# Kernel tuning notes

Measured on AMD Instinct MI355X. Metric: run time of the kernel, lower is better.

Reference implementation:

```python
import jax, jax.numpy as jnp
import numpy as np

N = 100000   # n_nodes
E = 1600000  # n_edges (avg degree 16)
IN, HID, OUT = 128, 128, 64


def setup_inputs() -> dict:
    key = jax.random.key(0)
    k0, k1, k2, k3 = jax.random.split(key, 4)
    x = jax.random.normal(k0, (N, IN), dtype=jnp.float32)
    edge_index = jax.random.randint(k1, (2, E), 0, N, dtype=jnp.int32)
    # Glorot-ish init for GCNConv weights, zero bias (PyG default bias=True)
    W1 = jax.random.normal(k2, (IN, HID), dtype=jnp.float32) * (1.0 / np.sqrt(IN))
    b1 = jnp.zeros((HID,), dtype=jnp.float32)
    W2 = jax.random.normal(k3, (HID, OUT), dtype=jnp.float32) * (1.0 / np.sqrt(HID))
    b2 = jnp.zeros((OUT,), dtype=jnp.float32)
    return {"x": x, "W1": W1, "b1": b1, "W2": W2, "b2": b2, "edge_index": edge_index}


def gcn_layer(x, W, b, src, dst):
    """PyG GCNConv: add self-loops, symmetric deg^{-1/2} normalization,
    linear transform, scatter-add aggregation at dst, plus bias."""
    n = x.shape[0]
    h = x @ W                                   # [n, d_out]
    loops = jnp.arange(n, dtype=src.dtype)
    s = jnp.concatenate([src, loops])           # sources incl. self-loops
    d = jnp.concatenate([dst, loops])           # targets incl. self-loops
    deg = jax.ops.segment_sum(jnp.ones_like(d, dtype=h.dtype), d, num_segments=n)
    dinv = jnp.where(deg > 0, jax.lax.rsqrt(deg), 0.0)
    norm = dinv[s] * dinv[d]                    # [E+n]
    msg = h[s] * norm[:, None]                  # gather + scale
    out = jax.ops.segment_sum(msg, d, num_segments=n)  # scatter-add
    return out + b


def reference(x, W1, b1, W2, b2, edge_index):
    src, dst = edge_index[0], edge_index[1]
    h = jax.nn.relu(gcn_layer(x, W1, b1, src, dst))
    return gcn_layer(h, W2, b2, src, dst)
```

## Files before the change

kernel.cpp:

```cpp
#include <hip/hip_runtime.h>

#define NNODES 100000
#define NEDGES 1600000
#define IND 128
#define HIDD 128
#define OUTD 64

#define BSHIFT 9
#define BSIZE  512
#define NBUCK  ((NNODES + BSIZE - 1) / BSIZE)
#define SLACK  9216
#define BIN_EPB  8192
#define SEG_CAP  10240
#define BINB   ((NEDGES + BIN_EPB - 1) / BIN_EPB)
#define WTB    ((IND * HIDD + HIDD * OUTD + 255) / 256)

typedef unsigned int  uint32;
typedef __attribute__((ext_vector_type(8))) short short8;
typedef __attribute__((ext_vector_type(4))) float floatx4;
typedef __attribute__((ext_vector_type(4))) unsigned int uivec4;
typedef __attribute__((ext_vector_type(4))) float fvec4;

__device__ __forceinline__ unsigned short f2bf(float f) {
    union { float f; uint32 u; } x; x.f = f;
    uint32 u = x.u;
    return (unsigned short)((u + 0x7fffu + ((u >> 16) & 1u)) >> 16);
}
__device__ __forceinline__ float bflo(uint32 u) {
    union { uint32 i; float f; } x; x.i = u << 16; return x.f;
}
__device__ __forceinline__ float bfhi(uint32 u) {
    union { uint32 i; float f; } x; x.i = u & 0xffff0000u; return x.f;
}

__global__ void k_bin(const int* __restrict__ src, const int* __restrict__ dst,
                      int* __restrict__ bcnt, uint32* __restrict__ staging, int e,
                      const float* __restrict__ W1, const float* __restrict__ W2,
                      unsigned short* __restrict__ wt1, unsigned short* __restrict__ wt2) {
    const int tid = threadIdx.x;
    if (blockIdx.x >= BINB) {
        int idx = (blockIdx.x - BINB) * 256 + tid;
        if (idx < IND * HIDD) {
            int k = idx / HIDD, m = idx - k * HIDD;
            wt1[m * IND + k] = f2bf(W1[idx]);
        } else {
            int j = idx - IND * HIDD;
            if (j < HIDD * OUTD) {
                int k = j / OUTD, m = j - k * OUTD;
                wt2[m * HIDD + k] = f2bf(W2[j]);
            }
        }
        return;
    }

    __shared__ int lh[NBUCK];
    __shared__ int lcur[NBUCK];
    for (int i = tid; i < NBUCK; i += 256) lh[i] = 0;
    __syncthreads();

    int start = blockIdx.x * BIN_EPB;
    int end = min(start + BIN_EPB, e);

    for (int i = start + tid; i < end; i += 256)
        atomicAdd(&lh[dst[i] >> BSHIFT], 1);
    __syncthreads();

    for (int i = tid; i < NBUCK; i += 256)
        lcur[i] = lh[i] ? atomicAdd(&bcnt[i], lh[i]) : 0;
    __syncthreads();

    for (int i = start + tid; i < end; i += 256) {
        int d = dst[i], s = src[i];
        int b = d >> BSHIFT;
        int pos = atomicAdd(&lcur[b], 1);
        if (pos < SLACK)
            staging[b * SLACK + pos] = ((uint32)(d & (BSIZE - 1)) << 17) | (uint32)s;
    }
}

__global__ void k_fill3(const uint32* __restrict__ staging, const int* __restrict__ bcnt,
                        int* __restrict__ row_ptr, int* __restrict__ csr_src,
                        float* __restrict__ dinv, int n) {
    __shared__ int nc[BSIZE];
    __shared__ int lcur[BSIZE];
    __shared__ int sbuf[256];
    __shared__ int boffl[NBUCK + 1];
    __shared__ int seg[SEG_CAP];
    const int b = blockIdx.x;
    const int base = b << BSHIFT;
    const int tid = threadIdx.x;
    const int nn = min(BSIZE, n - base);

    for (int i = tid; i < BSIZE; i += 256) nc[i] = 0;

    int vb = (tid < NBUCK) ? bcnt[tid] : 0;
    sbuf[tid] = vb;
    __syncthreads();
    for (int off = 1; off < 256; off <<= 1) {
        int t = (tid >= off) ? sbuf[tid - off] : 0;
        __syncthreads();
        sbuf[tid] += t;
        __syncthreads();
    }
    if (tid < NBUCK) boffl[tid] = sbuf[tid] - vb;
    if (tid == 255) boffl[NBUCK] = sbuf[255];
    __syncthreads();

    const uint32* st = staging + (size_t)b * SLACK;
    const int cnt = bcnt[b];
    for (int i = tid; i < cnt; i += 256)
        atomicAdd(&nc[st[i] >> 17], 1);
    __syncthreads();

    int a0 = nc[2 * tid], a1 = nc[2 * tid + 1];
    sbuf[tid] = a0 + a1;
    __syncthreads();
    for (int off = 1; off < 256; off <<= 1) {
        int t = (tid >= off) ? sbuf[tid - off] : 0;
        __syncthreads();
        sbuf[tid] += t;
        __syncthreads();
    }
    int ex = sbuf[tid] - (a0 + a1);
    const int r0 = boffl[b];
    if (2 * tid < nn) {
        row_ptr[base + 2 * tid] = r0 + ex;
        dinv[base + 2 * tid] = rsqrtf((float)(a0 + 1));
    }
    if (2 * tid + 1 < nn) {
        row_ptr[base + 2 * tid + 1] = r0 + ex + a0;
        dinv[base + 2 * tid + 1] = rsqrtf((float)(a1 + 1));
    }
    lcur[2 * tid] = ex;
    lcur[2 * tid + 1] = ex + a0;
    if (b == (int)gridDim.x - 1 && tid == 255) row_ptr[n] = boffl[NBUCK];
    __syncthreads();

    for (int i = tid; i < cnt; i += 256) {
        uint32 p = st[i];
        int dl = (int)(p >> 17);
        int s  = (int)(p & 0x1FFFFu);
        int pos = atomicAdd(&lcur[dl], 1);
        if (pos < SEG_CAP) seg[pos] = s;
        else               csr_src[r0 + pos] = s;
    }
    __syncthreads();
    int lim = min(cnt, SEG_CAP);
    for (int i = tid; i < lim; i += 256) csr_src[r0 + i] = seg[i];
}

template<int K, int M, bool ABF16>
__launch_bounds__(512)
__global__ void gemm_mfma(const void* __restrict__ Ap, const unsigned short* __restrict__ WT,
                          const float* __restrict__ dinv, unsigned short* __restrict__ C, int n) {
    constexpr int KP = K + 8;
    constexpr int NT = M / 16;
    __shared__ unsigned short Asl[128 * KP];
    __shared__ unsigned short Wsl[M * KP];

    const int tid = threadIdx.x;
    const int row0 = blockIdx.x * 128;

    {
        constexpr int SEG = (K * 2) / 16;
        const uint4* srcp = (const uint4*)WT;
        for (int idx = tid; idx < M * SEG; idx += 512) {
            int r = idx / SEG, s = idx - r * SEG;
            *(uint4*)(Wsl + r * KP + s * 8) = srcp[idx];
        }
    }
    if constexpr (ABF16) {
        constexpr int U4R = K / 8;
        const unsigned short* Ab = (const unsigned short*)Ap;
        for (int idx = tid; idx < 128 * U4R; idx += 512) {
            int r = idx / U4R, s = idx - r * U4R;
            int grow = row0 + r; if (grow >= n) grow = n - 1;
            *(uint4*)(Asl + r * KP + s * 8) = *(const uint4*)(Ab + (size_t)grow * K + s * 8);
        }
    } else {
        constexpr int F4R = K / 4;
        const float* Af = (const float*)Ap;
        for (int idx = tid; idx < 128 * F4R; idx += 512) {
            int r = idx / F4R, s = idx - r * F4R;
            int grow = row0 + r; if (grow >= n) grow = n - 1;
            float4 v = *(const float4*)(Af + (size_t)grow * K + s * 4);
            uint32 p0 = (uint32)f2bf(v.x) | ((uint32)f2bf(v.y) << 16);
            uint32 p1 = (uint32)f2bf(v.z) | ((uint32)f2bf(v.w) << 16);
            *(uint2*)(Asl + r * KP + s * 4) = make_uint2(p0, p1);
        }
    }
    __syncthreads();

    const int lane = tid & 63;
    const int wave = tid >> 6;
    const int mm = lane & 15;
    const int qq = lane >> 4;

    floatx4 acc[NT];
#pragma unroll
    for (int t = 0; t < NT; t++) acc[t] = (floatx4){0.f, 0.f, 0.f, 0.f};

#pragma unroll
    for (int kc = 0; kc < K / 32; kc++) {
        short8 a = *(const short8*)(Asl + (wave * 16 + mm) * KP + kc * 32 + qq * 8);
#pragma unroll
        for (int t = 0; t < NT; t++) {
            short8 b = *(const short8*)(Wsl + (t * 16 + mm) * KP + kc * 32 + qq * 8);
            acc[t] = __builtin_amdgcn_mfma_f32_16x16x32_bf16(a, b, acc[t], 0, 0, 0);
        }
    }

#pragma unroll
    for (int r = 0; r < 4; r++) {
        int grow = row0 + wave * 16 + qq * 4 + r;
        if (grow < n) {
            float dv = dinv[grow];
#pragma unroll
            for (int t = 0; t < NT; t++)
                C[(size_t)grow * M + t * 16 + mm] = f2bf(acc[t][r] * dv);
        }
    }
}

__launch_bounds__(256)
__global__ void gather_gemm(const unsigned short* __restrict__ h,
                            const int* __restrict__ row_ptr,
                            const int* __restrict__ csr_src,
                            const float* __restrict__ dinv,
                            const float* __restrict__ bias1,
                            const unsigned short* __restrict__ WT2,
                            unsigned short* __restrict__ C2, int n) {
    constexpr int K  = HIDD;
    constexpr int KP = K + 8;
    constexpr int M2 = OUTD;
    __shared__ unsigned short Atl[16 * KP];
    __shared__ unsigned short Wsl[M2 * KP];

    const int tid = threadIdx.x;

    {
        constexpr int SEG = (K * 2) / 16;
        const uint4* srcp = (const uint4*)WT2;
        for (int idx = tid; idx < M2 * SEG; idx += 256) {
            int r = idx / SEG, s = idx - r * SEG;
            *(uint4*)(Wsl + r * KP + s * 8) = srcp[idx];
        }
    }

    const int g = tid >> 4;
    const int l = tid & 15;
    const int v0 = blockIdx.x * 16;
    const int v = v0 + g;

    uint4 pk = make_uint4(0u, 0u, 0u, 0u);
    if (v < n) {
        const float dv = dinv[v];
        float acc[8];
        {
            uint4 u = *(const uint4*)(h + (size_t)v * K + l * 8);
            acc[0] = bflo(u.x); acc[1] = bfhi(u.x);
            acc[2] = bflo(u.y); acc[3] = bfhi(u.y);
            acc[4] = bflo(u.z); acc[5] = bfhi(u.z);
            acc[6] = bflo(u.w); acc[7] = bfhi(u.w);
        }

        int j   = row_ptr[v];
        int end = row_ptr[v + 1];
        for (; j + 3 < end; j += 4) {
            int s0 = csr_src[j];
            int s1 = csr_src[j + 1];
            int s2 = csr_src[j + 2];
            int s3 = csr_src[j + 3];
            uint4 u0 = *(const uint4*)(h + (size_t)s0 * K + l * 8);
            uint4 u1 = *(const uint4*)(h + (size_t)s1 * K + l * 8);
            uint4 u2 = *(const uint4*)(h + (size_t)s2 * K + l * 8);
            uint4 u3 = *(const uint4*)(h + (size_t)s3 * K + l * 8);
            acc[0] += (bflo(u0.x) + bflo(u1.x)) + (bflo(u2.x) + bflo(u3.x));
            acc[1] += (bfhi(u0.x) + bfhi(u1.x)) + (bfhi(u2.x) + bfhi(u3.x));
            acc[2] += (bflo(u0.y) + bflo(u1.y)) + (bflo(u2.y) + bflo(u3.y));
            acc[3] += (bfhi(u0.y) + bfhi(u1.y)) + (bfhi(u2.y) + bfhi(u3.y));
            acc[4] += (bflo(u0.z) + bflo(u1.z)) + (bflo(u2.z) + bflo(u3.z));
            acc[5] += (bfhi(u0.z) + bfhi(u1.z)) + (bfhi(u2.z) + bfhi(u3.z));
            acc[6] += (bflo(u0.w) + bflo(u1.w)) + (bflo(u2.w) + bflo(u3.w));
            acc[7] += (bfhi(u0.w) + bfhi(u1.w)) + (bfhi(u2.w) + bfhi(u3.w));
        }
        for (; j < end; j++) {
            int s0 = csr_src[j];
            uint4 u0 = *(const uint4*)(h + (size_t)s0 * K + l * 8);
            acc[0] += bflo(u0.x); acc[1] += bfhi(u0.x);
            acc[2] += bflo(u0.y); acc[3] += bfhi(u0.y);
            acc[4] += bflo(u0.z); acc[5] += bfhi(u0.z);
            acc[6] += bflo(u0.w); acc[7] += bfhi(u0.w);
        }

#pragma unroll
        for (int i = 0; i < 8; i++) {
            acc[i] = fmaxf(acc[i] * dv + bias1[l * 8 + i], 0.0f);
        }
        pk.x = (uint32)f2bf(acc[0]) | ((uint32)f2bf(acc[1]) << 16);
        pk.y = (uint32)f2bf(acc[2]) | ((uint32)f2bf(acc[3]) << 16);
        pk.z = (uint32)f2bf(acc[4]) | ((uint32)f2bf(acc[5]) << 16);
        pk.w = (uint32)f2bf(acc[6]) | ((uint32)f2bf(acc[7]) << 16);
    }
    *(uint4*)(Atl + g * KP + l * 8) = pk;
    __syncthreads();

    const int lane = tid & 63;
    const int wv = tid >> 6;
    const int mm = lane & 15;
    const int qq = lane >> 4;

    floatx4 o = (floatx4){0.f, 0.f, 0.f, 0.f};
#pragma unroll
    for (int kc = 0; kc < K / 32; kc++) {
        short8 a = *(const short8*)(Atl + mm * KP + kc * 32 + qq * 8);
        short8 b = *(const short8*)(Wsl + (wv * 16 + mm) * KP + kc * 32 + qq * 8);
        o = __builtin_amdgcn_mfma_f32_16x16x32_bf16(a, b, o, 0, 0, 0);
    }

#pragma unroll
    for (int r = 0; r < 4; r++) {
        int grow = v0 + qq * 4 + r;
        if (grow < n) {
            float dv2 = dinv[grow];
            C2[(size_t)grow * M2 + wv * 16 + mm] = f2bf(o[r] * dv2);
        }
    }
}

template<int M, bool RELU, bool OBF16>
__launch_bounds__(256)
__global__ void gather_k(const unsigned short* __restrict__ h,
                         const int* __restrict__ row_ptr,
                         const int* __restrict__ csr_src,
                         const float* __restrict__ dinv,
                         const float* __restrict__ bias,
                         void* __restrict__ outp, int n) {
    constexpr int LPG = M / 8;
    constexpr int GPB = 256 / LPG;
    const int g = threadIdx.x / LPG;
    const int l = threadIdx.x % LPG;
    const int v = blockIdx.x * GPB + g;
    if (v >= n) return;

    const float dv = dinv[v];
    float acc[8];
    {
        uint4 u = *(const uint4*)(h + (size_t)v * M + l * 8);
        acc[0] = bflo(u.x); acc[1] = bfhi(u.x);
        acc[2] = bflo(u.y); acc[3] = bfhi(u.y);
        acc[4] = bflo(u.z); acc[5] = bfhi(u.z);
        acc[6] = bflo(u.w); acc[7] = bfhi(u.w);
    }

    int j   = row_ptr[v];
    int end = row_ptr[v + 1];
    for (; j + 3 < end; j += 4) {
        int s0 = csr_src[j];
        int s1 = csr_src[j + 1];
        int s2 = csr_src[j + 2];
        int s3 = csr_src[j + 3];
        uint4 u0 = *(const uint4*)(h + (size_t)s0 * M + l * 8);
        uint4 u1 = *(const uint4*)(h + (size_t)s1 * M + l * 8);
        uint4 u2 = *(const uint4*)(h + (size_t)s2 * M + l * 8);
        uint4 u3 = *(const uint4*)(h + (size_t)s3 * M + l * 8);
        acc[0] += (bflo(u0.x) + bflo(u1.x)) + (bflo(u2.x) + bflo(u3.x));
        acc[1] += (bfhi(u0.x) + bfhi(u1.x)) + (bfhi(u2.x) + bfhi(u3.x));
        acc[2] += (bflo(u0.y) + bflo(u1.y)) + (bflo(u2.y) + bflo(u3.y));
        acc[3] += (bfhi(u0.y) + bfhi(u1.y)) + (bfhi(u2.y) + bfhi(u3.y));
        acc[4] += (bflo(u0.z) + bflo(u1.z)) + (bflo(u2.z) + bflo(u3.z));
        acc[5] += (bfhi(u0.z) + bfhi(u1.z)) + (bfhi(u2.z) + bfhi(u3.z));
        acc[6] += (bflo(u0.w) + bflo(u1.w)) + (bflo(u2.w) + bflo(u3.w));
        acc[7] += (bfhi(u0.w) + bfhi(u1.w)) + (bfhi(u2.w) + bfhi(u3.w));
    }
    for (; j < end; j++) {
        int s0 = csr_src[j];
        uint4 u0 = *(const uint4*)(h + (size_t)s0 * M + l * 8);
        acc[0] += bflo(u0.x); acc[1] += bfhi(u0.x);
        acc[2] += bflo(u0.y); acc[3] += bfhi(u0.y);
        acc[4] += bflo(u0.z); acc[5] += bfhi(u0.z);
        acc[6] += bflo(u0.w); acc[7] += bfhi(u0.w);
    }

#pragma unroll
    for (int i = 0; i < 8; i++) {
        acc[i] = acc[i] * dv + bias[l * 8 + i];
        if (RELU) acc[i] = fmaxf(acc[i], 0.0f);
    }

    if constexpr (OBF16) {
        uivec4 p;
#pragma unroll
        for (int c = 0; c < 4; c++)
            p[c] = (uint32)f2bf(acc[2 * c]) | ((uint32)f2bf(acc[2 * c + 1]) << 16);
        __builtin_nontemporal_store(p,
            (uivec4*)((unsigned short*)outp + (size_t)v * M + l * 8));
    } else {
        float* op = (float*)outp + (size_t)v * M + l * 8;
        fvec4 a0 = {acc[0], acc[1], acc[2], acc[3]};
        fvec4 a1 = {acc[4], acc[5], acc[6], acc[7]};
        __builtin_nontemporal_store(a0, (fvec4*)op);
        __builtin_nontemporal_store(a1, (fvec4*)(op + 4));
    }
}

extern "C" void kernel_launch(void* const* d_in, const int* in_sizes, int n_in,
                              void* d_out, int out_size, void* d_ws, size_t ws_size,
                              hipStream_t stream) {
    const float* x  = (const float*)d_in[0];
    const float* W1 = (const float*)d_in[1];
    const float* b1 = (const float*)d_in[2];
    const float* W2 = (const float*)d_in[3];
    const float* b2 = (const float*)d_in[4];
    const int*   ei = (const int*)d_in[5];
    const int* src = ei;
    const int* dst = ei + NEDGES;
    float* out = (float*)d_out;

    char* ws = (char*)d_ws;
    float*  dinv    = (float*)ws;   ws += (size_t)NNODES * 4;
    int*    row_ptr = (int*)ws;     ws += (size_t)(NNODES + 4) * 4;
    int*    bcnt    = (int*)ws;     ws += 256 * 4;
    int*    boff    = (int*)ws;     ws += 260 * 4;
    unsigned short* wt1 = (unsigned short*)ws;  ws += (size_t)IND * HIDD * 2;
    unsigned short* wt2 = (unsigned short*)ws;  ws += (size_t)HIDD * OUTD * 2;
    int*    csr_src = (int*)ws;     ws += (size_t)NEDGES * 4;
    uint32* staging = (uint32*)ws;  ws += (size_t)NBUCK * SLACK * 4;
    unsigned short* hbf1 = (unsigned short*)ws; ws += (size_t)NNODES * HIDD * 2;
    unsigned short* hbf2 = (unsigned short*)ws;

    hipMemsetAsync(bcnt, 0, 256 * 4, stream);
    k_bin<<<BINB + WTB, 256, 0, stream>>>(src, dst, bcnt, staging, NEDGES, W1, W2, wt1, wt2);
    k_fill3<<<NBUCK, 256, 0, stream>>>(staging, bcnt, row_ptr, csr_src, dinv, NNODES);

    gemm_mfma<IND, HIDD, false><<<(NNODES + 127) / 128, 512, 0, stream>>>(
        x, wt1, dinv, hbf1, NNODES);

    gather_gemm<<<(NNODES + 15) / 16, 256, 0, stream>>>(
        hbf1, row_ptr, csr_src, dinv, b1, wt2, hbf2, NNODES);

    gather_k<OUTD, false, false><<<(NNODES * (OUTD / 8) + 255) / 256, 256, 0, stream>>>(
        hbf2, row_ptr, csr_src, dinv, b2, out, NNODES);
}
```

Baseline: 306.9 us.

## Replace bucketed CSR build with global-atomic degree count and fuse scatter into GEMM

The two-pass bucket binning (staging buffer plus per-bucket shared-memory sort) is replaced by a per-node global atomic degree count, a block-wise row_ptr scan, and a cursor-based scatter into csr_src. The scatter blocks are launched in the same grid as the first-layer MFMA GEMM, so edge scatter overlaps the dense transform. This removes the staging buffer's write and re-read. In exchange it relies on heavily contended global atomics with random destinations, and the order of neighbours within each row becomes nondeterministic.

```diff
diff --git a/kernel.cpp b/kernel.cpp
--- a/kernel.cpp
+++ b/kernel.cpp
@@ -9,11 +9,14 @@
 #define BSHIFT 9
 #define BSIZE  512
 #define NBUCK  ((NNODES + BSIZE - 1) / BSIZE)
-#define SLACK  9216
-#define BIN_EPB  8192
-#define SEG_CAP  10240
-#define BINB   ((NEDGES + BIN_EPB - 1) / BIN_EPB)
+
+#define DEG_EPB 4096
+#define DEGB   ((NEDGES + DEG_EPB - 1) / DEG_EPB)
 #define WTB    ((IND * HIDD + HIDD * OUTD + 255) / 256)
+
+#define SCB    784
+#define SC_EPB ((NEDGES + SCB - 1) / SCB)
+#define GEMMB  ((NNODES + 127) / 128)
 
 typedef unsigned int  uint32;
 typedef __attribute__((ext_vector_type(8))) short short8;
@@ -33,13 +36,13 @@
     union { uint32 i; float f; } x; x.i = u & 0xffff0000u; return x.f;
 }
 
-__global__ void k_bin(const int* __restrict__ src, const int* __restrict__ dst,
-                      int* __restrict__ bcnt, uint32* __restrict__ staging, int e,
+__global__ void k_deg(const int* __restrict__ dst, int* __restrict__ deg,
+                      int* __restrict__ bsum, int e,
                       const float* __restrict__ W1, const float* __restrict__ W2,
                       unsigned short* __restrict__ wt1, unsigned short* __restrict__ wt2) {
     const int tid = threadIdx.x;
-    if (blockIdx.x >= BINB) {
-        int idx = (blockIdx.x - BINB) * 256 + tid;
+    if (blockIdx.x >= DEGB) {
+        int idx = (blockIdx.x - DEGB) * 256 + tid;
         if (idx < IND * HIDD) {
             int k = idx / HIDD, m = idx - k * HIDD;
             wt1[m * IND + k] = f2bf(W1[idx]);
@@ -54,112 +57,85 @@
     }
 
     __shared__ int lh[NBUCK];
-    __shared__ int lcur[NBUCK];
     for (int i = tid; i < NBUCK; i += 256) lh[i] = 0;
     __syncthreads();
 
-    int start = blockIdx.x * BIN_EPB;
-    int end = min(start + BIN_EPB, e);
-
-    for (int i = start + tid; i < end; i += 256)
-        atomicAdd(&lh[dst[i] >> BSHIFT], 1);
-    __syncthreads();
-
+    int start = blockIdx.x * DEG_EPB;
+    int end = min(start + DEG_EPB, e);
+    for (int i = start + tid; i < end; i += 256) {
+        int d = dst[i];
+        atomicAdd(&deg[d], 1);
+        atomicAdd(&lh[d >> BSHIFT], 1);
+    }
+    __syncthreads();
     for (int i = tid; i < NBUCK; i += 256)
-        lcur[i] = lh[i] ? atomicAdd(&bcnt[i], lh[i]) : 0;
-    __syncthreads();
-
-    for (int i = start + tid; i < end; i += 256) {
-        int d = dst[i], s = src[i];
-        int b = d >> BSHIFT;
-        int pos = atomicAdd(&lcur[b], 1);
-        if (pos < SLACK)
-            staging[b * SLACK + pos] = ((uint32)(d & (BSIZE - 1)) << 17) | (uint32)s;
-    }
-}
-
-__global__ void k_fill3(const uint32* __restrict__ staging, const int* __restrict__ bcnt,
-                        int* __restrict__ row_ptr, int* __restrict__ csr_src,
-                        float* __restrict__ dinv, int n) {
-    __shared__ int nc[BSIZE];
-    __shared__ int lcur[BSIZE];
-    __shared__ int sbuf[256];
-    __shared__ int boffl[NBUCK + 1];
-    __shared__ int seg[SEG_CAP];
+        if (lh[i]) atomicAdd(&bsum[i], lh[i]);
+}
+
+__global__ __launch_bounds__(512)
+void k_rowptr(const int* __restrict__ deg, const int* __restrict__ bsum,
+              int* __restrict__ row_ptr, int* __restrict__ cursor,
+              float* __restrict__ dinv, int n) {
+    __shared__ int sb[512];
     const int b = blockIdx.x;
-    const int base = b << BSHIFT;
     const int tid = threadIdx.x;
-    const int nn = min(BSIZE, n - base);
-
-    for (int i = tid; i < BSIZE; i += 256) nc[i] = 0;
-
-    int vb = (tid < NBUCK) ? bcnt[tid] : 0;
-    sbuf[tid] = vb;
-    __syncthreads();
-    for (int off = 1; off < 256; off <<= 1) {
-        int t = (tid >= off) ? sbuf[tid - off] : 0;
+
+    sb[tid] = (tid < b) ? bsum[tid] : 0;
+    __syncthreads();
+    for (int off = 256; off > 0; off >>= 1) {
+        if (tid < off) sb[tid] += sb[tid + off];
         __syncthreads();
-        sbuf[tid] += t;
+    }
+    const int base_off = sb[0];
+    __syncthreads();
+
+    const int v = (b << BSHIFT) + tid;
+    int dg = (v < n) ? deg[v] : 0;
+    sb[tid] = dg;
+    __syncthreads();
+    for (int off = 1; off < 512; off <<= 1) {
+        int t = (tid >= off) ? sb[tid - off] : 0;
         __syncthreads();
-    }
-    if (tid < NBUCK) boffl[tid] = sbuf[tid] - vb;
-    if (tid == 255) boffl[NBUCK] = sbuf[255];
-    __syncthreads();
-
-    const uint32* st = staging + (size_t)b * SLACK;
-    const int cnt = bcnt[b];
-    for (int i = tid; i < cnt; i += 256)
-        atomicAdd(&nc[st[i] >> 17], 1);
-    __syncthreads();
-
-    int a0 = nc[2 * tid], a1 = nc[2 * tid + 1];
-    sbuf[tid] = a0 + a1;
-    __syncthreads();
-    for (int off = 1; off < 256; off <<= 1) {
-        int t = (tid >= off) ? sbuf[tid - off] : 0;
+        sb[tid] += t;
         __syncthreads();
-        sbuf[tid] += t;
-        __syncthreads();
-    }
-    int ex = sbuf[tid] - (a0 + a1);
-    const int r0 = boffl[b];
-    if (2 * tid < nn) {
-        row_ptr[base + 2 * tid] = r0 + ex;
-        dinv[base + 2 * tid] = rsqrtf((float)(a0 + 1));
-    }
-    if (2 * tid + 1 < nn) {
-        row_ptr[base + 2 * tid + 1] = r0 + ex + a0;
-        dinv[base + 2 * tid + 1] = rsqrtf((float)(a1 + 1));
-    }
-    lcur[2 * tid] = ex;
-    lcur[2 * tid + 1] = ex + a0;
-    if (b == (int)gridDim.x - 1 && tid == 255) row_ptr[n] = boffl[NBUCK];
-    __syncthreads();
-
-    for (int i = tid; i < cnt; i += 256) {
-        uint32 p = st[i];
-        int dl = (int)(p >> 17);
-        int s  = (int)(p & 0x1FFFFu);
-        int pos = atomicAdd(&lcur[dl], 1);
-        if (pos < SEG_CAP) seg[pos] = s;
-        else               csr_src[r0 + pos] = s;
-    }
-    __syncthreads();
-    int lim = min(cnt, SEG_CAP);
-    for (int i = tid; i < lim; i += 256) csr_src[r0 + i] = seg[i];
-}
-
-template<int K, int M, bool ABF16>
+    }
+    int ex = sb[tid] - dg;
+    if (v < n) {
+        int rp = base_off + ex;
+        row_ptr[v] = rp;
+        cursor[v] = rp;
+        dinv[v] = rsqrtf((float)(dg + 1));
+        if (v == n - 1) row_ptr[n] = rp + dg;
+    }
+}
+
 __launch_bounds__(512)
-__global__ void gemm_mfma(const void* __restrict__ Ap, const unsigned short* __restrict__ WT,
-                          const float* __restrict__ dinv, unsigned short* __restrict__ C, int n) {
+__global__ void k_scatter_gemm(const int* __restrict__ src, const int* __restrict__ dst,
+                               int* __restrict__ cursor, int* __restrict__ csr_src, int e,
+                               const float* __restrict__ Af, const unsigned short* __restrict__ WT,
+                               const float* __restrict__ dinv, unsigned short* __restrict__ C, int n) {
+    constexpr int K = IND;
     constexpr int KP = K + 8;
+    constexpr int M = HIDD;
     constexpr int NT = M / 16;
     __shared__ unsigned short Asl[128 * KP];
     __shared__ unsigned short Wsl[M * KP];
 
     const int tid = threadIdx.x;
-    const int row0 = blockIdx.x * 128;
+    const int bid = blockIdx.x;
+
+    if (bid < SCB) {
+        int start = bid * SC_EPB;
+        int end = min(start + SC_EPB, e);
+        for (int i = start + tid; i < end; i += 512) {
+            int d = dst[i];
+            int pos = atomicAdd(&cursor[d], 1);
+            csr_src[pos] = src[i];
+        }
+        return;
+    }
+
+    const int row0 = (bid - SCB) * 128;
 
     {
         constexpr int SEG = (K * 2) / 16;
@@ -169,17 +145,8 @@
             *(uint4*)(Wsl + r * KP + s * 8) = srcp[idx];
         }
     }
-    if constexpr (ABF16) {
-        constexpr int U4R = K / 8;
-        const unsigned short* Ab = (const unsigned short*)Ap;
-        for (int idx = tid; idx < 128 * U4R; idx += 512) {
-            int r = idx / U4R, s = idx - r * U4R;
-            int grow = row0 + r; if (grow >= n) grow = n - 1;
-            *(uint4*)(Asl + r * KP + s * 8) = *(const uint4*)(Ab + (size_t)grow * K + s * 8);
-        }
-    } else {
+    {
         constexpr int F4R = K / 4;
-        const float* Af = (const float*)Ap;
         for (int idx = tid; idx < 128 * F4R; idx += 512) {
             int r = idx / F4R, s = idx - r * F4R;
             int grow = row0 + r; if (grow >= n) grow = n - 1;
@@ -420,21 +387,21 @@
     char* ws = (char*)d_ws;
     float*  dinv    = (float*)ws;   ws += (size_t)NNODES * 4;
     int*    row_ptr = (int*)ws;     ws += (size_t)(NNODES + 4) * 4;
-    int*    bcnt    = (int*)ws;     ws += 256 * 4;
-    int*    boff    = (int*)ws;     ws += 260 * 4;
+    int*    cursor  = (int*)ws;     ws += (size_t)NNODES * 4;
+    int*    deg     = (int*)ws;     ws += (size_t)NNODES * 4;
+    int*    bsum    = (int*)ws;     ws += 256 * 4;
     unsigned short* wt1 = (unsigned short*)ws;  ws += (size_t)IND * HIDD * 2;
     unsigned short* wt2 = (unsigned short*)ws;  ws += (size_t)HIDD * OUTD * 2;
     int*    csr_src = (int*)ws;     ws += (size_t)NEDGES * 4;
-    uint32* staging = (uint32*)ws;  ws += (size_t)NBUCK * SLACK * 4;
     unsigned short* hbf1 = (unsigned short*)ws; ws += (size_t)NNODES * HIDD * 2;
     unsigned short* hbf2 = (unsigned short*)ws;
 
-    hipMemsetAsync(bcnt, 0, 256 * 4, stream);
-    k_bin<<<BINB + WTB, 256, 0, stream>>>(src, dst, bcnt, staging, NEDGES, W1, W2, wt1, wt2);
-    k_fill3<<<NBUCK, 256, 0, stream>>>(staging, bcnt, row_ptr, csr_src, dinv, NNODES);
-
-    gemm_mfma<IND, HIDD, false><<<(NNODES + 127) / 128, 512, 0, stream>>>(
-        x, wt1, dinv, hbf1, NNODES);
+    hipMemsetAsync(deg, 0, (size_t)(NNODES + 256) * 4, stream);
+    k_deg<<<DEGB + WTB, 256, 0, stream>>>(dst, deg, bsum, NEDGES, W1, W2, wt1, wt2);
+    k_rowptr<<<NBUCK, 512, 0, stream>>>(deg, bsum, row_ptr, cursor, dinv, NNODES);
+
+    k_scatter_gemm<<<SCB + GEMMB, 512, 0, stream>>>(
+        src, dst, cursor, csr_src, NEDGES, x, wt1, dinv, hbf1, NNODES);
 
     gather_gemm<<<(NNODES + 15) / 16, 256, 0, stream>>>(
         hbf1, row_ptr, csr_src, dinv, b1, wt2, hbf2, NNODES);
```

Result: slower. 455.5 us (+48.4%).

## Fuse CSR fill with first GEMM via global degree atomics in binning

Applied to the files above, without the earlier changes.

The binning kernel now also counts per-node in-degree with global atomics, so the first GEMM can compute its deg^{-1/2} scaling directly instead of waiting for the CSR fill kernel. The CSR fill and the first GEMM are merged into one launch, with block ranges split between them and shared memory reused. The fill block size grows to 512 threads, one thread per node. This removes a kernel launch and a serialization point, letting fill and GEMM overlap, at the cost of 1.6M extra global atomics and a larger memset.

```diff
diff --git a/kernel.cpp b/kernel.cpp
--- a/kernel.cpp
+++ b/kernel.cpp
@@ -14,6 +14,7 @@
 #define SEG_CAP  10240
 #define BINB   ((NEDGES + BIN_EPB - 1) / BIN_EPB)
 #define WTB    ((IND * HIDD + HIDD * OUTD + 255) / 256)
+#define GEMMB  ((NNODES + 127) / 128)
 
 typedef unsigned int  uint32;
 typedef __attribute__((ext_vector_type(8))) short short8;
@@ -34,7 +35,8 @@
 }
 
 __global__ void k_bin(const int* __restrict__ src, const int* __restrict__ dst,
-                      int* __restrict__ bcnt, uint32* __restrict__ staging, int e,
+                      int* __restrict__ bcnt, int* __restrict__ deg,
+                      uint32* __restrict__ staging, int e,
                       const float* __restrict__ W1, const float* __restrict__ W2,
                       unsigned short* __restrict__ wt1, unsigned short* __restrict__ wt2) {
     const int tid = threadIdx.x;
@@ -61,8 +63,11 @@
     int start = blockIdx.x * BIN_EPB;
     int end = min(start + BIN_EPB, e);
 
-    for (int i = start + tid; i < end; i += 256)
-        atomicAdd(&lh[dst[i] >> BSHIFT], 1);
+    for (int i = start + tid; i < end; i += 256) {
+        int d = dst[i];
+        atomicAdd(&deg[d], 1);
+        atomicAdd(&lh[d >> BSHIFT], 1);
+    }
     __syncthreads();
 
     for (int i = tid; i < NBUCK; i += 256)
@@ -78,88 +83,88 @@
     }
 }
 
-__global__ void k_fill3(const uint32* __restrict__ staging, const int* __restrict__ bcnt,
-                        int* __restrict__ row_ptr, int* __restrict__ csr_src,
-                        float* __restrict__ dinv, int n) {
-    __shared__ int nc[BSIZE];
-    __shared__ int lcur[BSIZE];
-    __shared__ int sbuf[256];
-    __shared__ int boffl[NBUCK + 1];
-    __shared__ int seg[SEG_CAP];
-    const int b = blockIdx.x;
-    const int base = b << BSHIFT;
+__launch_bounds__(512)
+__global__ void k_fill_gemm(const uint32* __restrict__ staging, const int* __restrict__ bcnt,
+                            const int* __restrict__ deg,
+                            int* __restrict__ row_ptr, int* __restrict__ csr_src,
+                            float* __restrict__ dinv,
+                            const float* __restrict__ Af, const unsigned short* __restrict__ WT,
+                            unsigned short* __restrict__ C, int n) {
+    constexpr int K = IND;
+    constexpr int KP = K + 8;
+    constexpr int M = HIDD;
+    constexpr int NT = M / 16;
+    __shared__ __align__(16) char smem[(128 + 128) * KP * 2];
+
     const int tid = threadIdx.x;
-    const int nn = min(BSIZE, n - base);
-
-    for (int i = tid; i < BSIZE; i += 256) nc[i] = 0;
-
-    int vb = (tid < NBUCK) ? bcnt[tid] : 0;
-    sbuf[tid] = vb;
-    __syncthreads();
-    for (int off = 1; off < 256; off <<= 1) {
-        int t = (tid >= off) ? sbuf[tid - off] : 0;
-        __syncthreads();
-        sbuf[tid] += t;
-        __syncthreads();
-    }
-    if (tid < NBUCK) boffl[tid] = sbuf[tid] - vb;
-    if (tid == 255) boffl[NBUCK] = sbuf[255];
-    __syncthreads();
-
-    const uint32* st = staging + (size_t)b * SLACK;
-    const int cnt = bcnt[b];
-    for (int i = tid; i < cnt; i += 256)
-        atomicAdd(&nc[st[i] >> 17], 1);
-    __syncthreads();
-
-    int a0 = nc[2 * tid], a1 = nc[2 * tid + 1];
-    sbuf[tid] = a0 + a1;
-    __syncthreads();
-    for (int off = 1; off < 256; off <<= 1) {
-        int t = (tid >= off) ? sbuf[tid - off] : 0;
-        __syncthreads();
-        sbuf[tid] += t;
-        __syncthreads();
-    }
-    int ex = sbuf[tid] - (a0 + a1);
-    const int r0 = boffl[b];
-    if (2 * tid < nn) {
-        row_ptr[base + 2 * tid] = r0 + ex;
-        dinv[base + 2 * tid] = rsqrtf((float)(a0 + 1));
-    }
-    if (2 * tid + 1 < nn) {
-        row_ptr[base + 2 * tid + 1] = r0 + ex + a0;
-        dinv[base + 2 * tid + 1] = rsqrtf((float)(a1 + 1));
-    }
-    lcur[2 * tid] = ex;
-    lcur[2 * tid + 1] = ex + a0;
-    if (b == (int)gridDim.x - 1 && tid == 255) row_ptr[n] = boffl[NBUCK];
-    __syncthreads();
-
-    for (int i = tid; i < cnt; i += 256) {
-        uint32 p = st[i];
-        int dl = (int)(p >> 17);
-        int s  = (int)(p & 0x1FFFFu);
-        int pos = atomicAdd(&lcur[dl], 1);
-        if (pos < SEG_CAP) seg[pos] = s;
-        else               csr_src[r0 + pos] = s;
-    }
-    __syncthreads();
-    int lim = min(cnt, SEG_CAP);
-    for (int i = tid; i < lim; i += 256) csr_src[r0 + i] = seg[i];
-}
-
-template<int K, int M, bool ABF16>
-__launch_bounds__(512)
-__global__ void gemm_mfma(const void* __restrict__ Ap, const unsigned short* __restrict__ WT,
-                          const float* __restrict__ dinv, unsigned short* __restrict__ C, int n) {
-    constexpr int KP = K + 8;
-    constexpr int NT = M / 16;
-    __shared__ unsigned short Asl[128 * KP];
-    __shared__ unsigned short Wsl[M * KP];
-
-    const int tid = threadIdx.x;
-    const int row0 = blockIdx.x * 128;
+    const int bid = blockIdx.x;
+
+    if (bid < NBUCK) {
+        int* nc   = (int*)smem;
+        int* lcur = nc + 512;
+        int* sbuf = lcur + 512;
+        int* seg  = sbuf + 512;
+        const int b = bid;
+        const int base = b << BSHIFT;
+        const int v = base + tid;
+
+        nc[tid] = 0;
+
+        int vb = (tid < NBUCK) ? bcnt[tid] : 0;
+        sbuf[tid] = vb;
+        __syncthreads();
+        for (int off = 1; off < 512; off <<= 1) {
+            int t = (tid >= off) ? sbuf[tid - off] : 0;
+            __syncthreads();
+            sbuf[tid] += t;
+            __syncthreads();
+        }
+        const int r0    = (b > 0) ? sbuf[b - 1] : 0;
+        const int total = sbuf[NBUCK - 1];
+        __syncthreads();
+
+        const uint32* st = staging + (size_t)b * SLACK;
+        const int cnt = bcnt[b];
+        for (int i = tid; i < cnt; i += 512)
+            atomicAdd(&nc[st[i] >> 17], 1);
+        __syncthreads();
+
+        int dg = nc[tid];
+        sbuf[tid] = dg;
+        __syncthreads();
+        for (int off = 1; off < 512; off <<= 1) {
+            int t = (tid >= off) ? sbuf[tid - off] : 0;
+            __syncthreads();
+            sbuf[tid] += t;
+            __syncthreads();
+        }
+        int ex = sbuf[tid] - dg;
+        if (v < n) {
+            row_ptr[v] = r0 + ex;
+            dinv[v] = rsqrtf((float)(dg + 1));
+        }
+        lcur[tid] = ex;
+        if (b == NBUCK - 1 && tid == 0) row_ptr[n] = total;
+        __syncthreads();
+
+        for (int i = tid; i < cnt; i += 512) {
+            uint32 p = st[i];
+            int dl = (int)(p >> 17);
+            int s  = (int)(p & 0x1FFFFu);
+            int pos = atomicAdd(&lcur[dl], 1);
+            if (pos < SEG_CAP) seg[pos] = s;
+            else               csr_src[r0 + pos] = s;
+        }
+        __syncthreads();
+        int lim = min(cnt, SEG_CAP);
+        for (int i = tid; i < lim; i += 512) csr_src[r0 + i] = seg[i];
+        return;
+    }
+
+    unsigned short* Asl = (unsigned short*)smem;
+    unsigned short* Wsl = Asl + 128 * KP;
+
+    const int row0 = (bid - NBUCK) * 128;
 
     {
         constexpr int SEG = (K * 2) / 16;
@@ -169,17 +174,8 @@
             *(uint4*)(Wsl + r * KP + s * 8) = srcp[idx];
         }
     }
-    if constexpr (ABF16) {
-        constexpr int U4R = K / 8;
-        const unsigned short* Ab = (const unsigned short*)Ap;
-        for (int idx = tid; idx < 128 * U4R; idx += 512) {
-            int r = idx / U4R, s = idx - r * U4R;
-            int grow = row0 + r; if (grow >= n) grow = n - 1;
-            *(uint4*)(Asl + r * KP + s * 8) = *(const uint4*)(Ab + (size_t)grow * K + s * 8);
-        }
-    } else {
+    {
         constexpr int F4R = K / 4;
-        const float* Af = (const float*)Ap;
         for (int idx = tid; idx < 128 * F4R; idx += 512) {
             int r = idx / F4R, s = idx - r * F4R;
             int grow = row0 + r; if (grow >= n) grow = n - 1;
@@ -214,7 +210,7 @@
     for (int r = 0; r < 4; r++) {
         int grow = row0 + wave * 16 + qq * 4 + r;
         if (grow < n) {
-            float dv = dinv[grow];
+            float dv = rsqrtf((float)(deg[grow] + 1));
 #pragma unroll
             for (int t = 0; t < NT; t++)
                 C[(size_t)grow * M + t * 16 + mm] = f2bf(acc[t][r] * dv);
@@ -420,8 +416,8 @@
     char* ws = (char*)d_ws;
     float*  dinv    = (float*)ws;   ws += (size_t)NNODES * 4;
     int*    row_ptr = (int*)ws;     ws += (size_t)(NNODES + 4) * 4;
+    int*    deg     = (int*)ws;     ws += (size_t)NNODES * 4;
     int*    bcnt    = (int*)ws;     ws += 256 * 4;
-    int*    boff    = (int*)ws;     ws += 260 * 4;
     unsigned short* wt1 = (unsigned short*)ws;  ws += (size_t)IND * HIDD * 2;
     unsigned short* wt2 = (unsigned short*)ws;  ws += (size_t)HIDD * OUTD * 2;
     int*    csr_src = (int*)ws;     ws += (size_t)NEDGES * 4;
@@ -429,12 +425,11 @@
     unsigned short* hbf1 = (unsigned short*)ws; ws += (size_t)NNODES * HIDD * 2;
     unsigned short* hbf2 = (unsigned short*)ws;
 
-    hipMemsetAsync(bcnt, 0, 256 * 4, stream);
-    k_bin<<<BINB + WTB, 256, 0, stream>>>(src, dst, bcnt, staging, NEDGES, W1, W2, wt1, wt2);
-    k_fill3<<<NBUCK, 256, 0, stream>>>(staging, bcnt, row_ptr, csr_src, dinv, NNODES);
-
-    gemm_mfma<IND, HIDD, false><<<(NNODES + 127) / 128, 512, 0, stream>>>(
-        x, wt1, dinv, hbf1, NNODES);
+    hipMemsetAsync(deg, 0, (size_t)(NNODES + 256) * 4, stream);
+    k_bin<<<BINB + WTB, 256, 0, stream>>>(src, dst, bcnt, deg, staging, NEDGES, W1, W2, wt1, wt2);
+
+    k_fill_gemm<<<NBUCK + GEMMB, 512, 0, stream>>>(
+        staging, bcnt, deg, row_ptr, csr_src, dinv, x, wt1, hbf1, NNODES);
 
     gather_gemm<<<(NNODES + 15) / 16, 256, 0, stream>>>(
         hbf1, row_ptr, csr_src, dinv, b1, wt2, hbf2, NNODES);
```

Result: slower. 346.4 us (+12.9%).
